# Kernel optimization log

Hardware: AMD Instinct MI355X
Metric: run time of the kernel (lower is better)

Reference implementation:

```python
import jax, jax.numpy as jnp
import numpy as np

N_NODES, SEQ_LEN, IN_CH, HID, OUT_CH, N_EDGES = 10000, 12, 16, 64, 1, 160000


def setup_inputs() -> dict:
    key = jax.random.key(0)
    ks = jax.random.split(key, 16)
    s = 1.0 / np.sqrt(HID)
    u = lambda k, shape: jax.random.uniform(k, shape, jnp.float32, -s, s)
    return {
        "x_seq": jax.random.normal(ks[0], (1, SEQ_LEN, N_NODES, IN_CH), jnp.float32),
        "edge_index": jax.random.randint(ks[1], (2, N_EDGES), 0, N_NODES, jnp.int32),
        "gcn_w": jax.random.normal(ks[2], (IN_CH, HID), jnp.float32) / np.sqrt(IN_CH),
        "gcn_b": jnp.zeros((HID,), jnp.float32),
        "w_ih0": u(ks[3], (3 * HID, HID)),
        "w_hh0": u(ks[4], (3 * HID, HID)),
        "b_ih0": u(ks[5], (3 * HID,)),
        "b_hh0": u(ks[6], (3 * HID,)),
        "w_ih1": u(ks[7], (3 * HID, HID)),
        "w_hh1": u(ks[8], (3 * HID, HID)),
        "b_ih1": u(ks[9], (3 * HID,)),
        "b_hh1": u(ks[10], (3 * HID,)),
        "attn_w": u(ks[11], (HID, 1)),
        "attn_b": u(ks[12], (1,)),
        "fc_w": u(ks[13], (HID, OUT_CH)),
        "fc_b": u(ks[14], (OUT_CH,)),
    }


def _gcn_all_t(x_ntf, edge_index, w, b):
    # x_ntf: (N, T, F). Symmetric-normalized GCNConv with self loops (PyG default),
    # applied to every timestep at once (edge structure is static).
    n = x_ntf.shape[0]
    loop = jnp.arange(n, dtype=edge_index.dtype)
    src = jnp.concatenate([edge_index[0], loop])
    dst = jnp.concatenate([edge_index[1], loop])
    deg = jax.ops.segment_sum(jnp.ones_like(src, dtype=x_ntf.dtype), dst, num_segments=n)
    dis = jax.lax.rsqrt(deg)  # deg >= 1 thanks to self loops
    norm = dis[src] * dis[dst]  # (E+N,)
    msg = x_ntf[src] * norm[:, None, None]  # (E+N, T, F)
    agg = jax.ops.segment_sum(msg, dst, num_segments=n)  # (N, T, F)
    return agg @ w + b  # (N, T, H)


def _gru_layer(x, w_ih, w_hh, b_ih, b_hh):
    # x: (B, T, Hin) batch_first; PyTorch GRU cell equations, h0 = 0.
    bsz, _, _ = x.shape
    h_dim = w_hh.shape[1]
    xi = x @ w_ih.T + b_ih  # (B, T, 3H), precomputed input projections

    def step(h, xt):
        gh = h @ w_hh.T + b_hh
        ir, iz, in_ = jnp.split(xt, 3, axis=-1)
        hr, hz, hn = jnp.split(gh, 3, axis=-1)
        r = jax.nn.sigmoid(ir + hr)
        z = jax.nn.sigmoid(iz + hz)
        n = jnp.tanh(in_ + r * hn)
        h_new = (1.0 - z) * n + z * h
        return h_new, h_new

    h0 = jnp.zeros((bsz, h_dim), x.dtype)
    _, hs = jax.lax.scan(step, h0, jnp.swapaxes(xi, 0, 1))  # (T, B, H)
    return jnp.swapaxes(hs, 0, 1)


def reference(x_seq, edge_index, gcn_w, gcn_b, w_ih0, w_hh0, b_ih0, b_hh0,
              w_ih1, w_hh1, b_ih1, b_hh1, attn_w, attn_b, fc_w, fc_b):
    batch, seq_len, num_nodes, _ = x_seq.shape  # batch == 1 (see notes)
    # (B, T, N, F) -> (N, T, F)
    x_ntf = jnp.swapaxes(x_seq[0], 0, 1)
    gcn_out = jax.nn.relu(_gcn_all_t(x_ntf, edge_index, gcn_w, gcn_b))  # (N, T, H)
    # gru_input: (B*N, T, H); dropout between GRU layers disabled (inference)
    h1 = _gru_layer(gcn_out, w_ih0, w_hh0, b_ih0, b_hh0)
    gru_out = _gru_layer(h1, w_ih1, w_hh1, b_ih1, b_hh1)  # (N, T, H)
    attn_scores = jax.nn.softmax(gru_out @ attn_w + attn_b, axis=1)  # (N, T, 1)
    context = jnp.sum(attn_scores * gru_out, axis=1)  # (N, H)
    residual = (context @ fc_w + fc_b).reshape(batch, num_nodes, -1)
    last_known = x_seq[:, -1, :, 0][..., None]  # (B, N, 1)
    return last_known + residual
```

## Files before the change

kernel.cpp:

```cpp
#include <hip/hip_runtime.h>
#include <hip/hip_bf16.h>

#define N_NODES 10000
#define SEQ_T 12
#define IN_CH 16
#define HID 64
#define N_EDGES 160000
#define CAP 96
#define PB 0xAAAAAAAAu

typedef __attribute__((ext_vector_type(8))) short short8;
typedef __attribute__((ext_vector_type(4))) float floatx4;

__device__ __forceinline__ float frcp(float x){ return __builtin_amdgcn_rcpf(x); }
__device__ __forceinline__ float sigmf(float x){ return frcp(1.0f + __expf(-x)); }
__device__ __forceinline__ float tanh_fast(float x){ return 1.0f - 2.0f * frcp(1.0f + __expf(2.0f * x)); }
__device__ __forceinline__ unsigned short f2bf(float f){
  union { float f; unsigned int u; } c; c.f = f;
  unsigned int u = c.u;
  return (unsigned short)((u + 0x7FFFu + ((u >> 16) & 1u)) >> 16);
}
__device__ __forceinline__ unsigned short f2h(float f){
  _Float16 h = (_Float16)f; unsigned short u; __builtin_memcpy(&u, &h, 2); return u;
}
__device__ __forceinline__ float h2f(unsigned short u){
  _Float16 h; __builtin_memcpy(&h, &u, 2); return (float)h;
}
__device__ __forceinline__ void cvt4(ushort4 v, float* o){
  o[0] = h2f(v.x); o[1] = h2f(v.y); o[2] = h2f(v.z); o[3] = h2f(v.w);
}


__global__ void k_fill(const int* __restrict__ ei, unsigned int* __restrict__ cnt,
                       int* __restrict__ csr,
                       const float* __restrict__ wih0, const float* __restrict__ whh0,
                       const float* __restrict__ wih1, const float* __restrict__ whh1,
                       unsigned short* __restrict__ wF,
                       const float* __restrict__ x, unsigned short* __restrict__ xT){
  int i = blockIdx.x * 256 + threadIdx.x;
  if (i < 49152){
    const float* srcs[4] = {wih0, whh0, wih1, whh1};
    int p = i / 12288, ii = i - p * 12288;
    int e = ii & 7, l = (ii >> 3) & 63, jk = ii >> 9;
    int kt = jk / 12, jt = jk - kt * 12;
    int j = (l & 15) + 16 * jt;
    int k = ((l >> 4) * 8) + e + 32 * kt;
    wF[i] = f2bf(srcs[p][j * 64 + k]);
  }
  {
    int n = i >> 4, ch = i & 15;
    const float* xp = x + (size_t)n * IN_CH + ch;
    unsigned short tmp[SEQ_T];
    #pragma unroll
    for (int t = 0; t < SEQ_T; ++t) tmp[t] = f2h(xp[(size_t)t * N_NODES * IN_CH]);
    unsigned short* dp = xT + (size_t)n * 192 + ch * 12;
    *(ushort4*)(dp)     = make_ushort4(tmp[0], tmp[1], tmp[2],  tmp[3]);
    *(ushort4*)(dp + 4) = make_ushort4(tmp[4], tmp[5], tmp[6],  tmp[7]);
    *(ushort4*)(dp + 8) = make_ushort4(tmp[8], tmp[9], tmp[10], tmp[11]);
  }
  int s = ei[i], d = ei[N_EDGES + i];
  unsigned int pos = atomicAdd(&cnt[d], 1u) - PB;
  if (pos < CAP) csr[d * CAP + pos] = s;
}

__global__ __launch_bounds__(256, 3) void k_fused(
    const float* __restrict__ x, const unsigned short* __restrict__ xT,
    const unsigned int* __restrict__ cnt, const int* __restrict__ csr,
    const float* __restrict__ gcn_w, const float* __restrict__ gcn_b,
    const unsigned short* __restrict__ wF,
    const float* __restrict__ bih0, const float* __restrict__ bhh0,
    const float* __restrict__ bih1, const float* __restrict__ bhh1,
    const float* __restrict__ attn_w, const float* __restrict__ fc_w,
    const float* __restrict__ fc_b, float* __restrict__ out){
  __shared__ union {
    struct {
      float sm[SEQ_T][16][17];
      float smw[IN_CH * HID];
      float smb[HID];
      int2  eLDS[16][16];
    } A;
    struct {
      unsigned short HL[SEQ_T][1024];
      float scdc[SEQ_T][2][16];
    } B;
  } U;
  __shared__ union {
    unsigned short gout[SEQ_T][1024];
    unsigned short h1[2][1024];
  } V;

  const int tid = threadIdx.x;
  const int blk = blockIdx.x;

  {
    for (int i = tid; i < IN_CH * HID; i += 256) U.A.smw[i] = gcn_w[i];
    if (tid < HID) U.A.smb[tid] = gcn_b[tid];
    const int g = tid >> 4, ch = tid & 15;
    const int dst = blk * 16 + g;
    int deg = (int)(cnt[dst] - PB);
    if (deg > CAP) deg = CAP;
    float selfdis = rsqrtf((float)deg + 1.0f);
    float acc[SEQ_T];
    {
      const unsigned short* xs = xT + (size_t)dst * 192 + ch * 12;
      float f[SEQ_T];
      cvt4(*(const ushort4*)(xs),     f);
      cvt4(*(const ushort4*)(xs + 4), f + 4);
      cvt4(*(const ushort4*)(xs + 8), f + 8);
      #pragma unroll
      for (int t = 0; t < SEQ_T; ++t) acc[t] = selfdis * f[t];
    }
    for (int base = 0; base < deg; base += 16){
      int ep = base + ch;
      int2 ev = make_int2(0, 0);
      if (ep < deg){
        int s = csr[dst * CAP + ep];
        ev = make_int2(s, __float_as_int(rsqrtf((float)(cnt[s] - PB) + 1.0f)));
      }
      U.A.eLDS[g][ch] = ev;
      int c2 = deg - base; if (c2 > 16) c2 = 16;
      #pragma unroll 4
      for (int j = 0; j < c2; ++j){
        int2 e2 = U.A.eLDS[g][j];
        float wgt = __int_as_float(e2.y);
        const unsigned short* xp = xT + (size_t)e2.x * 192 + ch * 12;
        ushort4 va = *(const ushort4*)(xp);
        ushort4 vb = *(const ushort4*)(xp + 4);
        ushort4 vc = *(const ushort4*)(xp + 8);
        float f[SEQ_T];
        cvt4(va, f); cvt4(vb, f + 4); cvt4(vc, f + 8);
        #pragma unroll
        for (int t = 0; t < SEQ_T; ++t)
          acc[t] = fmaf(wgt, f[t], acc[t]);
      }
    }
    #pragma unroll
    for (int t = 0; t < SEQ_T; ++t) U.A.sm[t][g][ch] = selfdis * acc[t];
    __syncthreads();
    const int hq = tid & 15;
    float wreg[16][4];
    #pragma unroll
    for (int f = 0; f < 16; ++f)
      #pragma unroll
      for (int j = 0; j < 4; ++j) wreg[f][j] = U.A.smw[f * HID + hq * 4 + j];
    float b0 = U.A.smb[hq * 4],     b1 = U.A.smb[hq * 4 + 1],
          b2 = U.A.smb[hq * 4 + 2], b3 = U.A.smb[hq * 4 + 3];
    const int lb = (hq >> 3) * 512 + (g + 16 * ((hq >> 1) & 3)) * 8 + (hq & 1) * 4;
    #pragma unroll
    for (int t = 0; t < SEQ_T; ++t){
      float o0 = b0, o1 = b1, o2 = b2, o3 = b3;
      #pragma unroll
      for (int f = 0; f < 16; ++f){
        float v = U.A.sm[t][g][f];
        o0 = fmaf(v, wreg[f][0], o0);
        o1 = fmaf(v, wreg[f][1], o1);
        o2 = fmaf(v, wreg[f][2], o2);
        o3 = fmaf(v, wreg[f][3], o3);
      }
      ushort4 ov;
      ov.x = f2bf(fmaxf(o0, 0.0f));
      ov.y = f2bf(fmaxf(o1, 0.0f));
      ov.z = f2bf(fmaxf(o2, 0.0f));
      ov.w = f2bf(fmaxf(o3, 0.0f));
      *(ushort4*)(&V.gout[t][lb]) = ov;
    }
    __syncthreads();
  }

  const int w = tid >> 6;
  const int l = tid & 63;
  const int c = l & 15;
  const int q = l >> 4;
  const int hb = w * 16 + c;
  const int kt_h = hb >> 5;
  const int e_h = hb & 7;
  const int lf_h = 16 * ((hb >> 3) & 3);

  {
    float brz = bih0[hb] + bhh0[hb];
    float bzz = bih0[64 + hb] + bhh0[64 + hb];
    float bin = bih0[128 + hb], bhn = bhh0[128 + hb];
    short8 bw[2][3][2];
    #pragma unroll
    for (int g2 = 0; g2 < 2; ++g2)
      #pragma unroll
      for (int s = 0; s < 3; ++s)
        #pragma unroll
        for (int kt = 0; kt < 2; ++kt){
          int jt = w + 4 * s;
          size_t idx = ((((size_t)g2 * 2 + kt) * 12 + jt) * 64 + l) * 8;
          bw[g2][s][kt] = *(const short8*)(wF + idx);
        }
    float hp[4] = {0.f, 0.f, 0.f, 0.f};
    for (int t = 0; t < SEQ_T; ++t){
      short8 xa[2], ha[2];
      #pragma unroll
      for (int kt = 0; kt < 2; ++kt)
        xa[kt] = *(const short8*)&V.gout[t][kt * 512 + l * 8];
      if (t > 0){
        #pragma unroll
        for (int kt = 0; kt < 2; ++kt)
          ha[kt] = *(const short8*)&U.B.HL[t - 1][(kt * 64 + l) * 8];
      }
      floatx4 acc[2][3];
      #pragma unroll
      for (int g2 = 0; g2 < 2; ++g2)
        #pragma unroll
        for (int s = 0; s < 3; ++s) acc[g2][s] = (floatx4){0.f, 0.f, 0.f, 0.f};
      #pragma unroll
      for (int s = 0; s < 3; ++s)
        #pragma unroll
        for (int kt = 0; kt < 2; ++kt)
          acc[0][s] = __builtin_amdgcn_mfma_f32_16x16x32_bf16(xa[kt], bw[0][s][kt], acc[0][s], 0, 0, 0);
      if (t > 0){
        #pragma unroll
        for (int s = 0; s < 3; ++s)
          #pragma unroll
          for (int kt = 0; kt < 2; ++kt)
            acc[1][s] = __builtin_amdgcn_mfma_f32_16x16x32_bf16(ha[kt], bw[1][s][kt], acc[1][s], 0, 0, 0);
      }
      #pragma unroll
      for (int r = 0; r < 4; ++r){
        float rr = sigmf(acc[0][0][r] + acc[1][0][r] + brz);
        float zz = sigmf(acc[0][1][r] + acc[1][1][r] + bzz);
        float nn = tanh_fast(acc[0][2][r] + bin + rr * (acc[1][2][r] + bhn));
        float hn = (1.0f - zz) * nn + zz * hp[r];
        hp[r] = hn;
        U.B.HL[t][(kt_h * 64 + (q * 4 + r) + lf_h) * 8 + e_h] = f2bf(hn);
      }
      __syncthreads();
    }
  }

  short8 bwA[2];
  #pragma unroll
  for (int kt = 0; kt < 2; ++kt){
    short8 v;
    #pragma unroll
    for (int e = 0; e < 8; ++e){
      int k = q * 8 + e + 32 * kt;
      float f = (c == 0) ? attn_w[k] : (c == 1) ? fc_w[k] : 0.0f;
      v[e] = (short)f2bf(f);
    }
    bwA[kt] = v;
  }

  {
    float brz = bih1[hb] + bhh1[hb];
    float bzz = bih1[64 + hb] + bhh1[64 + hb];
    float bin = bih1[128 + hb], bhn = bhh1[128 + hb];
    short8 bw[2][3][2];
    #pragma unroll
    for (int g2 = 0; g2 < 2; ++g2)
      #pragma unroll
      for (int s = 0; s < 3; ++s)
        #pragma unroll
        for (int kt = 0; kt < 2; ++kt){
          int jt = w + 4 * s;
          size_t idx = ((((size_t)(2 + g2) * 2 + kt) * 12 + jt) * 64 + l) * 8;
          bw[g2][s][kt] = *(const short8*)(wF + idx);
        }
    float hp[4] = {0.f, 0.f, 0.f, 0.f};
    for (int t = 0; t < SEQ_T; ++t){
      int pr = t & 1;
      short8 xa[2], ha[2];
      #pragma unroll
      for (int kt = 0; kt < 2; ++kt)
        xa[kt] = *(const short8*)&U.B.HL[t][(kt * 64 + l) * 8];
      if (t > 0){
        #pragma unroll
        for (int kt = 0; kt < 2; ++kt)
          ha[kt] = *(const short8*)&V.h1[pr][(kt * 64 + l) * 8];
      }
      floatx4 acc[2][3];
      #pragma unroll
      for (int g2 = 0; g2 < 2; ++g2)
        #pragma unroll
        for (int s = 0; s < 3; ++s) acc[g2][s] = (floatx4){0.f, 0.f, 0.f, 0.f};
      #pragma unroll
      for (int s = 0; s < 3; ++s)
        #pragma unroll
        for (int kt = 0; kt < 2; ++kt)
          acc[0][s] = __builtin_amdgcn_mfma_f32_16x16x32_bf16(xa[kt], bw[0][s][kt], acc[0][s], 0, 0, 0);
      if (t > 0){
        #pragma unroll
        for (int s = 0; s < 3; ++s)
          #pragma unroll
          for (int kt = 0; kt < 2; ++kt)
            acc[1][s] = __builtin_amdgcn_mfma_f32_16x16x32_bf16(ha[kt], bw[1][s][kt], acc[1][s], 0, 0, 0);
      }
      if (w == 0 && t >= 1){
        floatx4 aA = (floatx4){0.f, 0.f, 0.f, 0.f};
        #pragma unroll
        for (int kt = 0; kt < 2; ++kt)
          aA = __builtin_amdgcn_mfma_f32_16x16x32_bf16(ha[kt], bwA[kt], aA, 0, 0, 0);
        if (c < 2){
          #pragma unroll
          for (int r = 0; r < 4; ++r) U.B.scdc[t - 1][c][q * 4 + r] = aA[r];
        }
      }
      #pragma unroll
      for (int r = 0; r < 4; ++r){
        float rr = sigmf(acc[0][0][r] + acc[1][0][r] + brz);
        float zz = sigmf(acc[0][1][r] + acc[1][1][r] + bzz);
        float nn = tanh_fast(acc[0][2][r] + bin + rr * (acc[1][2][r] + bhn));
        float hn = (1.0f - zz) * nn + zz * hp[r];
        hp[r] = hn;
        V.h1[1 - pr][(kt_h * 64 + (q * 4 + r) + lf_h) * 8 + e_h] = f2bf(hn);
      }
      __syncthreads();
    }
  }

  if (w == 0){
    short8 hL[2];
    #pragma unroll
    for (int kt = 0; kt < 2; ++kt)
      hL[kt] = *(const short8*)&V.h1[0][(kt * 64 + l) * 8];
    floatx4 aA = (floatx4){0.f, 0.f, 0.f, 0.f};
    #pragma unroll
    for (int kt = 0; kt < 2; ++kt)
      aA = __builtin_amdgcn_mfma_f32_16x16x32_bf16(hL[kt], bwA[kt], aA, 0, 0, 0);
    if (c < 2){
      #pragma unroll
      for (int r = 0; r < 4; ++r) U.B.scdc[SEQ_T - 1][c][q * 4 + r] = aA[r];
    }
    int gn = blk * 16 + l;
    if (l < 16){
      float sc[SEQ_T], dc[SEQ_T];
      #pragma unroll
      for (int t = 0; t < SEQ_T; ++t){ sc[t] = U.B.scdc[t][0][l]; dc[t] = U.B.scdc[t][1][l]; }
      float m = sc[0];
      #pragma unroll
      for (int t = 1; t < SEQ_T; ++t) m = fmaxf(m, sc[t]);
      float den = 0.0f, num = 0.0f;
      #pragma unroll
      for (int t = 0; t < SEQ_T; ++t){
        float p = __expf(sc[t] - m);
        den += p;
        num = fmaf(p, dc[t], num);
      }
      float y = fc_b[0] + num * frcp(den);
      float last = x[((size_t)(SEQ_T - 1) * N_NODES + gn) * IN_CH];
      out[gn] = last + y;
    }
  }
}

extern "C" void kernel_launch(void* const* d_in, const int* in_sizes, int n_in,
                              void* d_out, int out_size, void* d_ws, size_t ws_size,
                              hipStream_t stream){
  const float* x = (const float*)d_in[0];
  const int* ei  = (const int*)d_in[1];
  char* ws = (char*)d_ws;
  unsigned int*   cnt = (unsigned int*)(ws);
  int*            csr = (int*)(ws + 40960);
  unsigned short* wF  = (unsigned short*)(ws + 3880960);
  unsigned short* xT  = (unsigned short*)(ws + 3979264);

  k_fill<<<625, 256, 0, stream>>>(ei, cnt, csr,
      (const float*)d_in[4], (const float*)d_in[5],
      (const float*)d_in[8], (const float*)d_in[9], wF,
      x, xT);
  k_fused<<<625, 256, 0, stream>>>(
      x, xT, cnt, csr,
      (const float*)d_in[2], (const float*)d_in[3], wF,
      (const float*)d_in[6],  (const float*)d_in[7],
      (const float*)d_in[10], (const float*)d_in[11],
      (const float*)d_in[12], (const float*)d_in[14], (const float*)d_in[15],
      (float*)d_out);
}
```

Baseline: 141.2 us.

## Transpose GRU MFMA operands, pad hidden-state LDS layout, use packed fp16/bf16 math

The GRU MFMA calls swap their A and B operands, so each lane now holds four consecutive hidden units for a single node. Hidden states are written as one packed 8-byte store into a padded [16][72] LDS layout, replacing scattered 2-byte stores. Biases are folded into the accumulator initial values, and the gate blend is rewritten to save an operation. The GCN gather now accumulates in packed half2 FMAs instead of converting to fp32, which reduces conversion and ALU work but risks precision loss on nodes with high degree.

```diff
diff --git a/kernel.cpp b/kernel.cpp
--- a/kernel.cpp
+++ b/kernel.cpp
@@ -1,5 +1,6 @@
 #include <hip/hip_runtime.h>
 #include <hip/hip_bf16.h>
+#include <hip/hip_fp16.h>
 
 #define N_NODES 10000
 #define SEQ_T 12
@@ -23,11 +24,10 @@
 __device__ __forceinline__ unsigned short f2h(float f){
   _Float16 h = (_Float16)f; unsigned short u; __builtin_memcpy(&u, &h, 2); return u;
 }
-__device__ __forceinline__ float h2f(unsigned short u){
-  _Float16 h; __builtin_memcpy(&h, &u, 2); return (float)h;
-}
-__device__ __forceinline__ void cvt4(ushort4 v, float* o){
-  o[0] = h2f(v.x); o[1] = h2f(v.y); o[2] = h2f(v.z); o[3] = h2f(v.w);
+__device__ __forceinline__ unsigned int cvt_pk_bf16(float a, float b){
+  unsigned int r;
+  asm("v_cvt_pk_bf16_f32 %0, %1, %2" : "=v"(r) : "v"(a), "v"(b));
+  return r;
 }
 
 
@@ -80,13 +80,13 @@
       int2  eLDS[16][16];
     } A;
     struct {
-      unsigned short HL[SEQ_T][1024];
+      unsigned short HL[SEQ_T][16][72];
       float scdc[SEQ_T][2][16];
     } B;
   } U;
   __shared__ union {
     unsigned short gout[SEQ_T][1024];
-    unsigned short h1[2][1024];
+    unsigned short h1[2][16][72];
   } V;
 
   const int tid = threadIdx.x;
@@ -100,15 +100,12 @@
     int deg = (int)(cnt[dst] - PB);
     if (deg > CAP) deg = CAP;
     float selfdis = rsqrtf((float)deg + 1.0f);
-    float acc[SEQ_T];
+    __half2 ah[6];
     {
-      const unsigned short* xs = xT + (size_t)dst * 192 + ch * 12;
-      float f[SEQ_T];
-      cvt4(*(const ushort4*)(xs),     f);
-      cvt4(*(const ushort4*)(xs + 4), f + 4);
-      cvt4(*(const ushort4*)(xs + 8), f + 8);
-      #pragma unroll
-      for (int t = 0; t < SEQ_T; ++t) acc[t] = selfdis * f[t];
+      const __half2* xs = (const __half2*)(const void*)(xT + (size_t)dst * 192 + ch * 12);
+      __half2 sd2 = __float2half2_rn(selfdis);
+      #pragma unroll
+      for (int k = 0; k < 6; ++k) ah[k] = __hmul2(sd2, xs[k]);
     }
     for (int base = 0; base < deg; base += 16){
       int ep = base + ch;
@@ -122,20 +119,17 @@
       #pragma unroll 4
       for (int j = 0; j < c2; ++j){
         int2 e2 = U.A.eLDS[g][j];
-        float wgt = __int_as_float(e2.y);
-        const unsigned short* xp = xT + (size_t)e2.x * 192 + ch * 12;
-        ushort4 va = *(const ushort4*)(xp);
-        ushort4 vb = *(const ushort4*)(xp + 4);
-        ushort4 vc = *(const ushort4*)(xp + 8);
-        float f[SEQ_T];
-        cvt4(va, f); cvt4(vb, f + 4); cvt4(vc, f + 8);
+        __half2 wh = __float2half2_rn(__int_as_float(e2.y));
+        const __half2* xp = (const __half2*)(const void*)(xT + (size_t)e2.x * 192 + ch * 12);
         #pragma unroll
-        for (int t = 0; t < SEQ_T; ++t)
-          acc[t] = fmaf(wgt, f[t], acc[t]);
-      }
-    }
-    #pragma unroll
-    for (int t = 0; t < SEQ_T; ++t) U.A.sm[t][g][ch] = selfdis * acc[t];
+        for (int k = 0; k < 6; ++k) ah[k] = __hfma2(wh, xp[k], ah[k]);
+      }
+    }
+    #pragma unroll
+    for (int t = 0; t < SEQ_T; ++t){
+      float f = (t & 1) ? __high2float(ah[t >> 1]) : __low2float(ah[t >> 1]);
+      U.A.sm[t][g][ch] = selfdis * f;
+    }
     __syncthreads();
     const int hq = tid & 15;
     float wreg[16][4];
@@ -157,12 +151,9 @@
         o2 = fmaf(v, wreg[f][2], o2);
         o3 = fmaf(v, wreg[f][3], o3);
       }
-      ushort4 ov;
-      ov.x = f2bf(fmaxf(o0, 0.0f));
-      ov.y = f2bf(fmaxf(o1, 0.0f));
-      ov.z = f2bf(fmaxf(o2, 0.0f));
-      ov.w = f2bf(fmaxf(o3, 0.0f));
-      *(ushort4*)(&V.gout[t][lb]) = ov;
+      unsigned int plo = cvt_pk_bf16(fmaxf(o0, 0.0f), fmaxf(o1, 0.0f));
+      unsigned int phi = cvt_pk_bf16(fmaxf(o2, 0.0f), fmaxf(o3, 0.0f));
+      *(uint2*)(void*)(&V.gout[t][lb]) = make_uint2(plo, phi);
     }
     __syncthreads();
   }
@@ -171,15 +162,17 @@
   const int l = tid & 63;
   const int c = l & 15;
   const int q = l >> 4;
-  const int hb = w * 16 + c;
-  const int kt_h = hb >> 5;
-  const int e_h = hb & 7;
-  const int lf_h = 16 * ((hb >> 3) & 3);
+  const int hbase = 16 * w + 4 * q;
 
   {
-    float brz = bih0[hb] + bhh0[hb];
-    float bzz = bih0[64 + hb] + bhh0[64 + hb];
-    float bin = bih0[128 + hb], bhn = bhh0[128 + hb];
+    floatx4 brz4, bzz4, bin4, bhn4;
+    #pragma unroll
+    for (int r = 0; r < 4; ++r){
+      brz4[r] = bih0[hbase + r] + bhh0[hbase + r];
+      bzz4[r] = bih0[64 + hbase + r] + bhh0[64 + hbase + r];
+      bin4[r] = bih0[128 + hbase + r];
+      bhn4[r] = bhh0[128 + hbase + r];
+    }
     short8 bw[2][3][2];
     #pragma unroll
     for (int g2 = 0; g2 < 2; ++g2)
@@ -193,41 +186,36 @@
         }
     float hp[4] = {0.f, 0.f, 0.f, 0.f};
     for (int t = 0; t < SEQ_T; ++t){
-      short8 xa[2], ha[2];
-      #pragma unroll
-      for (int kt = 0; kt < 2; ++kt)
-        xa[kt] = *(const short8*)&V.gout[t][kt * 512 + l * 8];
+      short8 xa0 = *(const short8*)&V.gout[t][l * 8];
+      short8 xa1 = *(const short8*)&V.gout[t][512 + l * 8];
+      floatx4 aR = brz4, aZ = bzz4, aNx = bin4, aNh = bhn4;
       if (t > 0){
-        #pragma unroll
-        for (int kt = 0; kt < 2; ++kt)
-          ha[kt] = *(const short8*)&U.B.HL[t - 1][(kt * 64 + l) * 8];
-      }
-      floatx4 acc[2][3];
-      #pragma unroll
-      for (int g2 = 0; g2 < 2; ++g2)
-        #pragma unroll
-        for (int s = 0; s < 3; ++s) acc[g2][s] = (floatx4){0.f, 0.f, 0.f, 0.f};
-      #pragma unroll
-      for (int s = 0; s < 3; ++s)
-        #pragma unroll
-        for (int kt = 0; kt < 2; ++kt)
-          acc[0][s] = __builtin_amdgcn_mfma_f32_16x16x32_bf16(xa[kt], bw[0][s][kt], acc[0][s], 0, 0, 0);
-      if (t > 0){
-        #pragma unroll
-        for (int s = 0; s < 3; ++s)
-          #pragma unroll
-          for (int kt = 0; kt < 2; ++kt)
-            acc[1][s] = __builtin_amdgcn_mfma_f32_16x16x32_bf16(ha[kt], bw[1][s][kt], acc[1][s], 0, 0, 0);
-      }
+        short8 ha0 = *(const short8*)&U.B.HL[t - 1][c][8 * q];
+        short8 ha1 = *(const short8*)&U.B.HL[t - 1][c][8 * q + 32];
+        aR  = __builtin_amdgcn_mfma_f32_16x16x32_bf16(bw[1][0][0], ha0, aR, 0, 0, 0);
+        aR  = __builtin_amdgcn_mfma_f32_16x16x32_bf16(bw[1][0][1], ha1, aR, 0, 0, 0);
+        aZ  = __builtin_amdgcn_mfma_f32_16x16x32_bf16(bw[1][1][0], ha0, aZ, 0, 0, 0);
+        aZ  = __builtin_amdgcn_mfma_f32_16x16x32_bf16(bw[1][1][1], ha1, aZ, 0, 0, 0);
+        aNh = __builtin_amdgcn_mfma_f32_16x16x32_bf16(bw[1][2][0], ha0, aNh, 0, 0, 0);
+        aNh = __builtin_amdgcn_mfma_f32_16x16x32_bf16(bw[1][2][1], ha1, aNh, 0, 0, 0);
+      }
+      aR  = __builtin_amdgcn_mfma_f32_16x16x32_bf16(bw[0][0][0], xa0, aR, 0, 0, 0);
+      aR  = __builtin_amdgcn_mfma_f32_16x16x32_bf16(bw[0][0][1], xa1, aR, 0, 0, 0);
+      aZ  = __builtin_amdgcn_mfma_f32_16x16x32_bf16(bw[0][1][0], xa0, aZ, 0, 0, 0);
+      aZ  = __builtin_amdgcn_mfma_f32_16x16x32_bf16(bw[0][1][1], xa1, aZ, 0, 0, 0);
+      aNx = __builtin_amdgcn_mfma_f32_16x16x32_bf16(bw[0][2][0], xa0, aNx, 0, 0, 0);
+      aNx = __builtin_amdgcn_mfma_f32_16x16x32_bf16(bw[0][2][1], xa1, aNx, 0, 0, 0);
+      float h4[4];
       #pragma unroll
       for (int r = 0; r < 4; ++r){
-        float rr = sigmf(acc[0][0][r] + acc[1][0][r] + brz);
-        float zz = sigmf(acc[0][1][r] + acc[1][1][r] + bzz);
-        float nn = tanh_fast(acc[0][2][r] + bin + rr * (acc[1][2][r] + bhn));
-        float hn = (1.0f - zz) * nn + zz * hp[r];
-        hp[r] = hn;
-        U.B.HL[t][(kt_h * 64 + (q * 4 + r) + lf_h) * 8 + e_h] = f2bf(hn);
-      }
+        float rr = sigmf(aR[r]);
+        float zz = sigmf(aZ[r]);
+        float nn = tanh_fast(aNx[r] + rr * aNh[r]);
+        h4[r] = nn + zz * (hp[r] - nn);
+        hp[r] = h4[r];
+      }
+      *(uint2*)(void*)(&U.B.HL[t][c][hbase]) =
+          make_uint2(cvt_pk_bf16(h4[0], h4[1]), cvt_pk_bf16(h4[2], h4[3]));
       __syncthreads();
     }
   }
@@ -246,9 +234,14 @@
   }
 
   {
-    float brz = bih1[hb] + bhh1[hb];
-    float bzz = bih1[64 + hb] + bhh1[64 + hb];
-    float bin = bih1[128 + hb], bhn = bhh1[128 + hb];
+    floatx4 brz4, bzz4, bin4, bhn4;
+    #pragma unroll
+    for (int r = 0; r < 4; ++r){
+      brz4[r] = bih1[hbase + r] + bhh1[hbase + r];
+      bzz4[r] = bih1[64 + hbase + r] + bhh1[64 + hbase + r];
+      bin4[r] = bih1[128 + hbase + r];
+      bhn4[r] = bhh1[128 + hbase + r];
+    }
     short8 bw[2][3][2];
     #pragma unroll
     for (int g2 = 0; g2 < 2; ++g2)
@@ -263,67 +256,58 @@
     float hp[4] = {0.f, 0.f, 0.f, 0.f};
     for (int t = 0; t < SEQ_T; ++t){
       int pr = t & 1;
-      short8 xa[2], ha[2];
-      #pragma unroll
-      for (int kt = 0; kt < 2; ++kt)
-        xa[kt] = *(const short8*)&U.B.HL[t][(kt * 64 + l) * 8];
+      short8 xa0 = *(const short8*)&U.B.HL[t][c][8 * q];
+      short8 xa1 = *(const short8*)&U.B.HL[t][c][8 * q + 32];
+      floatx4 aR = brz4, aZ = bzz4, aNx = bin4, aNh = bhn4;
       if (t > 0){
-        #pragma unroll
-        for (int kt = 0; kt < 2; ++kt)
-          ha[kt] = *(const short8*)&V.h1[pr][(kt * 64 + l) * 8];
-      }
-      floatx4 acc[2][3];
-      #pragma unroll
-      for (int g2 = 0; g2 < 2; ++g2)
-        #pragma unroll
-        for (int s = 0; s < 3; ++s) acc[g2][s] = (floatx4){0.f, 0.f, 0.f, 0.f};
-      #pragma unroll
-      for (int s = 0; s < 3; ++s)
-        #pragma unroll
-        for (int kt = 0; kt < 2; ++kt)
-          acc[0][s] = __builtin_amdgcn_mfma_f32_16x16x32_bf16(xa[kt], bw[0][s][kt], acc[0][s], 0, 0, 0);
-      if (t > 0){
-        #pragma unroll
-        for (int s = 0; s < 3; ++s)
-          #pragma unroll
-          for (int kt = 0; kt < 2; ++kt)
-            acc[1][s] = __builtin_amdgcn_mfma_f32_16x16x32_bf16(ha[kt], bw[1][s][kt], acc[1][s], 0, 0, 0);
-      }
-      if (w == 0 && t >= 1){
-        floatx4 aA = (floatx4){0.f, 0.f, 0.f, 0.f};
-        #pragma unroll
-        for (int kt = 0; kt < 2; ++kt)
-          aA = __builtin_amdgcn_mfma_f32_16x16x32_bf16(ha[kt], bwA[kt], aA, 0, 0, 0);
-        if (c < 2){
-          #pragma unroll
-          for (int r = 0; r < 4; ++r) U.B.scdc[t - 1][c][q * 4 + r] = aA[r];
+        short8 ha0 = *(const short8*)&V.h1[pr][c][8 * q];
+        short8 ha1 = *(const short8*)&V.h1[pr][c][8 * q + 32];
+        aR  = __builtin_amdgcn_mfma_f32_16x16x32_bf16(bw[1][0][0], ha0, aR, 0, 0, 0);
+        aR  = __builtin_amdgcn_mfma_f32_16x16x32_bf16(bw[1][0][1], ha1, aR, 0, 0, 0);
+        aZ  = __builtin_amdgcn_mfma_f32_16x16x32_bf16(bw[1][1][0], ha0, aZ, 0, 0, 0);
+        aZ  = __builtin_amdgcn_mfma_f32_16x16x32_bf16(bw[1][1][1], ha1, aZ, 0, 0, 0);
+        aNh = __builtin_amdgcn_mfma_f32_16x16x32_bf16(bw[1][2][0], ha0, aNh, 0, 0, 0);
+        aNh = __builtin_amdgcn_mfma_f32_16x16x32_bf16(bw[1][2][1], ha1, aNh, 0, 0, 0);
+        if (w == 0){
+          floatx4 aA = (floatx4){0.f, 0.f, 0.f, 0.f};
+          aA = __builtin_amdgcn_mfma_f32_16x16x32_bf16(bwA[0], ha0, aA, 0, 0, 0);
+          aA = __builtin_amdgcn_mfma_f32_16x16x32_bf16(bwA[1], ha1, aA, 0, 0, 0);
+          if (q == 0){
+            U.B.scdc[t - 1][0][c] = aA[0];
+            U.B.scdc[t - 1][1][c] = aA[1];
+          }
         }
       }
+      aR  = __builtin_amdgcn_mfma_f32_16x16x32_bf16(bw[0][0][0], xa0, aR, 0, 0, 0);
+      aR  = __builtin_amdgcn_mfma_f32_16x16x32_bf16(bw[0][0][1], xa1, aR, 0, 0, 0);
+      aZ  = __builtin_amdgcn_mfma_f32_16x16x32_bf16(bw[0][1][0], xa0, aZ, 0, 0, 0);
+      aZ  = __builtin_amdgcn_mfma_f32_16x16x32_bf16(bw[0][1][1], xa1, aZ, 0, 0, 0);
+      aNx = __builtin_amdgcn_mfma_f32_16x16x32_bf16(bw[0][2][0], xa0, aNx, 0, 0, 0);
+      aNx = __builtin_amdgcn_mfma_f32_16x16x32_bf16(bw[0][2][1], xa1, aNx, 0, 0, 0);
+      float h4[4];
       #pragma unroll
       for (int r = 0; r < 4; ++r){
-        float rr = sigmf(acc[0][0][r] + acc[1][0][r] + brz);
-        float zz = sigmf(acc[0][1][r] + acc[1][1][r] + bzz);
-        float nn = tanh_fast(acc[0][2][r] + bin + rr * (acc[1][2][r] + bhn));
-        float hn = (1.0f - zz) * nn + zz * hp[r];
-        hp[r] = hn;
-        V.h1[1 - pr][(kt_h * 64 + (q * 4 + r) + lf_h) * 8 + e_h] = f2bf(hn);
-      }
+        float rr = sigmf(aR[r]);
+        float zz = sigmf(aZ[r]);
+        float nn = tanh_fast(aNx[r] + rr * aNh[r]);
+        h4[r] = nn + zz * (hp[r] - nn);
+        hp[r] = h4[r];
+      }
+      *(uint2*)(void*)(&V.h1[1 - pr][c][hbase]) =
+          make_uint2(cvt_pk_bf16(h4[0], h4[1]), cvt_pk_bf16(h4[2], h4[3]));
       __syncthreads();
     }
   }
 
   if (w == 0){
-    short8 hL[2];
-    #pragma unroll
-    for (int kt = 0; kt < 2; ++kt)
-      hL[kt] = *(const short8*)&V.h1[0][(kt * 64 + l) * 8];
+    short8 hL0 = *(const short8*)&V.h1[0][c][8 * q];
+    short8 hL1 = *(const short8*)&V.h1[0][c][8 * q + 32];
     floatx4 aA = (floatx4){0.f, 0.f, 0.f, 0.f};
-    #pragma unroll
-    for (int kt = 0; kt < 2; ++kt)
-      aA = __builtin_amdgcn_mfma_f32_16x16x32_bf16(hL[kt], bwA[kt], aA, 0, 0, 0);
-    if (c < 2){
-      #pragma unroll
-      for (int r = 0; r < 4; ++r) U.B.scdc[SEQ_T - 1][c][q * 4 + r] = aA[r];
+    aA = __builtin_amdgcn_mfma_f32_16x16x32_bf16(bwA[0], hL0, aA, 0, 0, 0);
+    aA = __builtin_amdgcn_mfma_f32_16x16x32_bf16(bwA[1], hL1, aA, 0, 0, 0);
+    if (q == 0){
+      U.B.scdc[SEQ_T - 1][0][c] = aA[0];
+      U.B.scdc[SEQ_T - 1][1][c] = aA[1];
     }
     int gn = blk * 16 + l;
     if (l < 16){
```

After: 138.0 us. 1.02x faster.
